# Performance work log

Hardware: AMD Instinct MI355X
Metric: run time of the kernel (lower is better)

## Reference

```python
import jax, jax.numpy as jnp
import numpy as np

N_NODES = 50000
N_EDGES = 800000
NUM_MOL = 2000
MSG_PASSES = 4


def setup_inputs() -> dict:
    key = jax.random.key(0)
    ks = jax.random.split(key, 16)
    x = jax.random.randint(ks[0], (N_NODES,), 0, 119)
    edge_attr = jax.random.randint(ks[1], (N_EDGES,), 0, 4)
    edge_index = jax.random.randint(ks[2], (2, N_EDGES), 0, N_NODES)
    batch = jnp.sort(jax.random.randint(ks[3], (N_NODES,), 0, NUM_MOL))
    f32 = jnp.float32
    return {
        "x": x,
        "edge_attr": edge_attr,
        "edge_index": edge_index,
        "batch": batch,
        "atom_table": jax.random.normal(ks[4], (119, 128), f32) * 0.1,
        "bond_table": jax.random.normal(ks[5], (4, 64), f32) * 0.1,
        "Wi": jax.random.normal(ks[6], (192, 128), f32) * 0.05,
        "bi": jax.random.normal(ks[7], (128,), f32) * 0.01,
        "Wu1": jax.random.normal(ks[8], (320, 128), f32) * 0.05,
        "bu1": jax.random.normal(ks[9], (128,), f32) * 0.01,
        "Wu2": jax.random.normal(ks[10], (128, 128), f32) * 0.05,
        "bu2": jax.random.normal(ks[11], (128,), f32) * 0.01,
        "Wr1": jax.random.normal(ks[12], (128, 512), f32) * 0.05,
        "br1": jax.random.normal(ks[13], (512,), f32) * 0.01,
        "Wr2": jax.random.normal(ks[14], (512, 1), f32) * 0.05,
        "br2": jax.random.normal(ks[15], (1,), f32) * 0.01,
    }


def reference(x, edge_attr, edge_index, batch,
              atom_table, bond_table, Wi, bi, Wu1, bu1, Wu2, bu2,
              Wr1, br1, Wr2, br2):
    atom = atom_table[x]                      # [N, atom_emb]
    bond = bond_table[edge_attr]              # [E, bond_emb]
    src, dst = edge_index[0], edge_index[1]
    a_src = atom[src]                         # [E, atom_emb]
    ab = jnp.concatenate([a_src, bond], axis=1)  # [E, atom_emb+bond_emb]
    msg = jax.nn.relu(ab @ Wi + bi)           # [E, msg_dim]
    for _ in range(MSG_PASSES):
        agg = jax.ops.segment_sum(msg, dst, num_segments=N_NODES)  # [N, msg_dim]
        upd_in = jnp.concatenate([ab, agg[src]], axis=1)           # [E, 320]
        h = jax.nn.relu(upd_in @ Wu1 + bu1)
        msg = jax.nn.relu(h @ Wu2 + bu2)
    node_state = jax.ops.segment_sum(msg, dst, num_segments=N_NODES)
    mol_state = jax.ops.segment_sum(node_state, batch, num_segments=NUM_MOL)
    out = jax.nn.relu(mol_state @ Wr1 + br1) @ Wr2 + br2  # [NUM_MOL, 1]
    return jnp.squeeze(out, axis=-1)
```

## Files before the change

kernel.cpp:

```cpp
#include <hip/hip_runtime.h>
#include <hip/hip_bf16.h>

#define N_NODES 50000
#define N_EDGES 800000
#define NUM_MOL 2000

typedef __attribute__((ext_vector_type(8))) short short8;
typedef __attribute__((ext_vector_type(4))) float f32x4;

union bfbits { __hip_bfloat16 b; short s; };

__global__ void k_tables(const float* __restrict__ atom_table,
                         const float* __restrict__ bond_table,
                         const float* __restrict__ Wi,
                         const float* __restrict__ bi,
                         const float* __restrict__ Wu1,
                         const float* __restrict__ bu1,
                         float* __restrict__ T1, float* __restrict__ U1,
                         float* __restrict__ T2c, float* __restrict__ U2c) {
  int b = blockIdx.x;
  int c = threadIdx.x;
  if (b < 119) {
    float t = 0.f, u = 0.f;
    for (int k = 0; k < 128; k++) {
      float a = atom_table[b * 128 + k];
      t += a * Wi[k * 128 + c];
      u += a * Wu1[k * 128 + c];
    }
    T1[b * 128 + c] = t;
    U1[b * 128 + c] = u;
  } else {
    int a = b - 119;
    float t = bi[c], u = bu1[c];
    for (int k = 0; k < 64; k++) {
      float bv = bond_table[a * 64 + k];
      t += bv * Wi[(128 + k) * 128 + c];
      u += bv * Wu1[(128 + k) * 128 + c];
    }
    T2c[a * 128 + c] = t;
    U2c[a * 128 + c] = u;
  }
}

__global__ void k_tt(const float* __restrict__ T1, const float* __restrict__ T2c,
                     float* __restrict__ TT) {
  int r = blockIdx.x;
  int c = threadIdx.x;
  float v = T1[(r >> 2) * 128 + c] + T2c[(r & 3) * 128 + c];
  TT[r * 128 + c] = v > 0.f ? v : 0.f;
}

__global__ void k_wt2(const float* __restrict__ Wu2, const float* __restrict__ Wu1,
                      short* __restrict__ Wt, short* __restrict__ Wlo,
                      short* __restrict__ W1t, short* __restrict__ W1lo) {
  int b = blockIdx.x;
  int k = threadIdx.x;
  if (b < 128) {
    float w = Wu2[k * 128 + b];
    bfbits hi; hi.b = __float2bfloat16(w);
    float hf = __bfloat162float(hi.b);
    bfbits lo; lo.b = __float2bfloat16(w - hf);
    Wt[b * 128 + k] = hi.s;
    Wlo[b * 128 + k] = lo.s;
  } else {
    int n = b - 128;
    float w = Wu1[(192 + k) * 128 + n];
    bfbits hi; hi.b = __float2bfloat16(w);
    float hf = __bfloat162float(hi.b);
    bfbits lo; lo.b = __float2bfloat16(w - hf);
    W1t[n * 128 + k] = hi.s;
    W1lo[n * 128 + k] = lo.s;
  }
}

__global__ void k_u1x(const int* __restrict__ x, const float* __restrict__ U1,
                      float* __restrict__ D_) {
  int n = blockIdx.x * 4 + (threadIdx.x >> 6);
  int lane = threadIdx.x & 63;
  int xn = x[n];
  float2 v = *(const float2*)&U1[xn * 128 + lane * 2];
  *(float2*)&D_[n * 128 + lane * 2] = v;
}

__global__ void k_fillb(const int* __restrict__ eidx, const int* __restrict__ attr,
                        const int* __restrict__ x,
                        int* __restrict__ cnt, int* __restrict__ csr1) {
  int e = blockIdx.x * 256 + threadIdx.x;
  int d = eidx[N_EDGES + e];
  int s = eidx[e];
  int a = attr[e];
  int pos = atomicAdd(&cnt[d], 1);
  if (pos < 64) {
    int packed = (s * 4 + a) | ((x[s] * 4 + a) << 18);
    __builtin_nontemporal_store(packed, &csr1[d * 64 + pos]);
  }
}

__global__ void k_molptr(const int* __restrict__ batch, int* __restrict__ molptr) {
  int m = blockIdx.x * 256 + threadIdx.x;
  if (m > NUM_MOL) return;
  int lo = 0, hi = N_NODES;
  while (lo < hi) {
    int mid = (lo + hi) >> 1;
    if (batch[mid] < m) lo = mid + 1; else hi = mid;
  }
  molptr[m] = lo;
}

__global__ void k_gather0(const int* __restrict__ cnt, const int* __restrict__ csr1,
                          const float* __restrict__ TT, float* __restrict__ A_) {
  int n = blockIdx.x * 4 + (threadIdx.x >> 6);
  int lane = threadIdx.x & 63;
  int g = lane >> 5;
  int p = lane & 31;
  int beg = n * 64;
  int end = beg + cnt[n];
  float s0 = 0.f, s1 = 0.f, s2 = 0.f, s3 = 0.f;
  int i = beg;
  for (; i + 3 < end; i += 4) {
    int idxA = ((unsigned)csr1[i + g]) >> 18;
    int idxB = ((unsigned)csr1[i + 2 + g]) >> 18;
    float4 va = *(const float4*)&TT[idxA * 128 + p * 4];
    float4 vb = *(const float4*)&TT[idxB * 128 + p * 4];
    s0 += va.x + vb.x; s1 += va.y + vb.y;
    s2 += va.z + vb.z; s3 += va.w + vb.w;
  }
  for (; i < end; i += 2) {
    if (i + g < end) {
      int idx = ((unsigned)csr1[i + g]) >> 18;
      float4 v = *(const float4*)&TT[idx * 128 + p * 4];
      s0 += v.x; s1 += v.y; s2 += v.z; s3 += v.w;
    }
  }
  s0 += __shfl_xor(s0, 32, 64);
  s1 += __shfl_xor(s1, 32, 64);
  s2 += __shfl_xor(s2, 32, 64);
  s3 += __shfl_xor(s3, 32, 64);
  float2 o;
  o.x = (g == 0) ? s0 : s2;
  o.y = (g == 0) ? s1 : s3;
  *(float2*)&A_[n * 128 + p * 4 + g * 2] = o;
}

__global__ void k_gather(const int* __restrict__ cnt, const int* __restrict__ csr1,
                         const __hip_bfloat16* __restrict__ M, float* __restrict__ A_) {
  int n = blockIdx.x * 4 + (threadIdx.x >> 6);
  int lane = threadIdx.x & 63;
  int g = lane >> 4;
  int p = lane & 15;
  int beg = n * 64;
  int end = beg + cnt[n];
  float s[8];
#pragma unroll
  for (int j = 0; j < 8; j++) s[j] = 0.f;
  const short* Ms = (const short*)M;
  int i = beg;
  for (; i + 7 < end; i += 8) {
    int idxA = csr1[i + g] & 0x3FFFF;
    int idxB = csr1[i + 4 + g] & 0x3FFFF;
    short8 va = *(const short8*)&Ms[idxA * 128 + p * 8];
    short8 vb = *(const short8*)&Ms[idxB * 128 + p * 8];
#pragma unroll
    for (int j = 0; j < 4; j++) {
      float2 fa = __bfloat1622float2(*(const __hip_bfloat162*)&((const short*)&va)[j * 2]);
      float2 fb = __bfloat1622float2(*(const __hip_bfloat162*)&((const short*)&vb)[j * 2]);
      s[j * 2] += fa.x + fb.x;
      s[j * 2 + 1] += fa.y + fb.y;
    }
  }
  for (; i < end; i += 4) {
    if (i + g < end) {
      int idx = csr1[i + g] & 0x3FFFF;
      short8 va = *(const short8*)&Ms[idx * 128 + p * 8];
#pragma unroll
      for (int j = 0; j < 4; j++) {
        float2 fa = __bfloat1622float2(*(const __hip_bfloat162*)&((const short*)&va)[j * 2]);
        s[j * 2] += fa.x;
        s[j * 2 + 1] += fa.y;
      }
    }
  }
#pragma unroll
  for (int j = 0; j < 8; j++) s[j] += __shfl_xor(s[j], 16, 64);
#pragma unroll
  for (int j = 0; j < 8; j++) s[j] += __shfl_xor(s[j], 32, 64);
  float2 o;
  o.x = s[g * 2];
  o.y = s[g * 2 + 1];
  *(float2*)&A_[n * 128 + p * 8 + g * 2] = o;
}

__global__ __launch_bounds__(256, 2) void k_mm1m(const float* __restrict__ A_,
                                                 const short* __restrict__ W1t,
                                                 const short* __restrict__ W1lo,
                                                 const float* __restrict__ D_,
                                                 float* __restrict__ B2_) {
  __shared__ float mbuf[4][16][68];
  int t = threadIdx.x;
  int lane = t & 63;
  int m = lane & 15;
  int quad = lane >> 4;
  int wslot = t >> 6;
  int w0 = blockIdx.x * 4 + wslot;
  int h = w0 & 1;

  short8 whi[4][4], wlo[4][4];
#pragma unroll
  for (int kc = 0; kc < 4; kc++)
#pragma unroll
    for (int nt = 0; nt < 4; nt++) {
      int n = h * 64 + nt * 16 + m;
      whi[kc][nt] = *(const short8*)&W1t[n * 128 + kc * 32 + quad * 8];
      wlo[kc][nt] = *(const short8*)&W1lo[n * 128 + kc * 32 + quad * 8];
    }

  for (int tid = w0; tid < 6250; tid += 4096) {
    int s = tid >> 1;
    int row = s * 16 + m;
    f32x4 acc[4];
#pragma unroll
    for (int nt = 0; nt < 4; nt++) acc[nt] = (f32x4){0.f, 0.f, 0.f, 0.f};

#pragma unroll
    for (int kc = 0; kc < 4; kc++) {
      int k0 = kc * 32 + quad * 8;
      short8 ahi, alo;
      {
        float av[8];
        *(float4*)&av[0] = *(const float4*)&A_[row * 128 + k0];
        *(float4*)&av[4] = *(const float4*)&A_[row * 128 + k0 + 4];
#pragma unroll
        for (int j = 0; j < 8; j++) {
          float hv = av[j];
          bfbits hi; hi.b = __float2bfloat16(hv);
          float hf = __bfloat162float(hi.b);
          bfbits lo; lo.b = __float2bfloat16(hv - hf);
          ahi[j] = hi.s;
          alo[j] = lo.s;
        }
      }
#pragma unroll
      for (int nt = 0; nt < 4; nt++) {
        acc[nt] = __builtin_amdgcn_mfma_f32_16x16x32_bf16(ahi, whi[kc][nt], acc[nt], 0, 0, 0);
        acc[nt] = __builtin_amdgcn_mfma_f32_16x16x32_bf16(alo, whi[kc][nt], acc[nt], 0, 0, 0);
        acc[nt] = __builtin_amdgcn_mfma_f32_16x16x32_bf16(ahi, wlo[kc][nt], acc[nt], 0, 0, 0);
      }
    }

#pragma unroll
    for (int nt = 0; nt < 4; nt++)
#pragma unroll
      for (int r = 0; r < 4; r++)
        mbuf[wslot][quad * 4 + r][nt * 16 + m] = acc[nt][r];
#pragma unroll
    for (int p = 0; p < 4; p++) {
      int c = p * 64 + lane;
      int rr = c >> 4;
      int qf = c & 15;
      int n = s * 16 + rr;
      float4 v = *(const float4*)&mbuf[wslot][rr][qf * 4];
      float4 d = *(const float4*)&D_[n * 128 + h * 64 + qf * 4];
      v.x += d.x; v.y += d.y; v.z += d.z; v.w += d.w;
      *(float4*)&B2_[n * 128 + h * 64 + qf * 4] = v;
    }
  }
}

__global__ __launch_bounds__(256, 2) void k_mm2(const float* __restrict__ B2_,
                                                const float* __restrict__ U2c,
                                                const short* __restrict__ Wt,
                                                const short* __restrict__ Wlo,
                                                const float* __restrict__ bu2,
                                                __hip_bfloat16* __restrict__ M) {
  __shared__ short mbuf[4][16][68];
  int t = threadIdx.x;
  int lane = t & 63;
  int m = lane & 15;
  int quad = lane >> 4;
  int wslot = t >> 6;
  int w0 = blockIdx.x * 4 + wslot;
  int h = w0 & 1;

  short8 whi[4][4], wlo[4][4];
#pragma unroll
  for (int kc = 0; kc < 4; kc++)
#pragma unroll
    for (int nt = 0; nt < 4; nt++) {
      int n = h * 64 + nt * 16 + m;
      whi[kc][nt] = *(const short8*)&Wt[n * 128 + kc * 32 + quad * 8];
      wlo[kc][nt] = *(const short8*)&Wlo[n * 128 + kc * 32 + quad * 8];
    }
  float bias[4];
#pragma unroll
  for (int nt = 0; nt < 4; nt++) bias[nt] = bu2[h * 64 + nt * 16 + m];

  for (int tid = w0; tid < 25000; tid += 4096) {
    int s = tid >> 1;
    int node = s * 4 + (m >> 2);
    int attr = m & 3;
    f32x4 acc[4];
#pragma unroll
    for (int nt = 0; nt < 4; nt++) acc[nt] = (f32x4){0.f, 0.f, 0.f, 0.f};

#pragma unroll
    for (int kc = 0; kc < 4; kc++) {
      int k0 = kc * 32 + quad * 8;
      short8 ahi, alo;
      {
        float bba[8], u2a[8];
        *(float4*)&bba[0] = *(const float4*)&B2_[node * 128 + k0];
        *(float4*)&bba[4] = *(const float4*)&B2_[node * 128 + k0 + 4];
        *(float4*)&u2a[0] = *(const float4*)&U2c[attr * 128 + k0];
        *(float4*)&u2a[4] = *(const float4*)&U2c[attr * 128 + k0 + 4];
#pragma unroll
        for (int j = 0; j < 8; j++) {
          float hv = bba[j] + u2a[j];
          hv = hv > 0.f ? hv : 0.f;
          bfbits hi; hi.b = __float2bfloat16(hv);
          float hf = __bfloat162float(hi.b);
          bfbits lo; lo.b = __float2bfloat16(hv - hf);
          ahi[j] = hi.s;
          alo[j] = lo.s;
        }
      }
#pragma unroll
      for (int nt = 0; nt < 4; nt++) {
        acc[nt] = __builtin_amdgcn_mfma_f32_16x16x32_bf16(ahi, whi[kc][nt], acc[nt], 0, 0, 0);
        acc[nt] = __builtin_amdgcn_mfma_f32_16x16x32_bf16(alo, whi[kc][nt], acc[nt], 0, 0, 0);
        acc[nt] = __builtin_amdgcn_mfma_f32_16x16x32_bf16(ahi, wlo[kc][nt], acc[nt], 0, 0, 0);
      }
    }

#pragma unroll
    for (int nt = 0; nt < 4; nt++) {
#pragma unroll
      for (int r = 0; r < 4; r++) {
        float v = acc[nt][r] + bias[nt];
        v = v > 0.f ? v : 0.f;
        bfbits o; o.b = __float2bfloat16(v);
        mbuf[wslot][quad * 4 + r][nt * 16 + m] = o.s;
      }
    }
    {
      int rr = lane >> 2;
      int qq = lane & 3;
      short8 v = *(const short8*)&mbuf[wslot][rr][qq * 8];
      *(short8*)((short*)M + (s * 16 + rr) * 128 + h * 64 + qq * 8) = v;
      short8 v2 = *(const short8*)&mbuf[wslot][rr][(qq + 4) * 8];
      *(short8*)((short*)M + (s * 16 + rr) * 128 + h * 64 + (qq + 4) * 8) = v2;
    }
  }
}

__global__ void k_molgather(const float* __restrict__ A_, const int* __restrict__ molptr,
                            float* __restrict__ mol) {
  int m = blockIdx.x * 4 + (threadIdx.x >> 6);
  int lane = threadIdx.x & 63;
  int beg = molptr[m], end = molptr[m + 1];
  float ax = 0.f, ay = 0.f;
  int n = beg;
  for (; n + 1 < end; n += 2) {
    float2 v0 = *(const float2*)&A_[n * 128 + lane * 2];
    float2 v1 = *(const float2*)&A_[(n + 1) * 128 + lane * 2];
    ax += v0.x + v1.x;
    ay += v0.y + v1.y;
  }
  if (n < end) {
    float2 v0 = *(const float2*)&A_[n * 128 + lane * 2];
    ax += v0.x;
    ay += v0.y;
  }
  float2 o; o.x = ax; o.y = ay;
  *(float2*)&mol[m * 128 + lane * 2] = o;
}

__global__ __launch_bounds__(256) void k_readout(const float* __restrict__ mol,
                                                 const float* __restrict__ Wr1,
                                                 const float* __restrict__ br1,
                                                 const float* __restrict__ Wr2,
                                                 const float* __restrict__ br2,
                                                 float* __restrict__ out) {
  int m = blockIdx.x;
  __shared__ float ms[128];
  __shared__ float red[256];
  int t = threadIdx.x;
  if (t < 128) ms[t] = mol[m * 128 + t];
  __syncthreads();
  float part = 0.f;
#pragma unroll
  for (int jj = 0; jj < 2; jj++) {
    int j = t + jj * 256;
    float acc = br1[j];
#pragma unroll
    for (int k = 0; k < 128; k += 4) {
      float4 m4 = *(const float4*)&ms[k];
      acc += m4.x * Wr1[k * 512 + j] + m4.y * Wr1[(k + 1) * 512 + j] +
             m4.z * Wr1[(k + 2) * 512 + j] + m4.w * Wr1[(k + 3) * 512 + j];
    }
    acc = acc > 0.f ? acc : 0.f;
    part += acc * Wr2[j];
  }
  red[t] = part;
  __syncthreads();
  for (int s = 128; s > 0; s >>= 1) {
    if (t < s) red[t] += red[t + s];
    __syncthreads();
  }
  if (t == 0) out[m] = red[0] + br2[0];
}

extern "C" void kernel_launch(void* const* d_in, const int* in_sizes, int n_in,
                              void* d_out, int out_size, void* d_ws, size_t ws_size,
                              hipStream_t stream) {
  const int* x        = (const int*)d_in[0];
  const int* eattr    = (const int*)d_in[1];
  const int* eidx     = (const int*)d_in[2];
  const int* batch    = (const int*)d_in[3];
  const float* atom_table = (const float*)d_in[4];
  const float* bond_table = (const float*)d_in[5];
  const float* Wi  = (const float*)d_in[6];
  const float* bi  = (const float*)d_in[7];
  const float* Wu1 = (const float*)d_in[8];
  const float* bu1 = (const float*)d_in[9];
  const float* Wu2 = (const float*)d_in[10];
  const float* bu2 = (const float*)d_in[11];
  const float* Wr1 = (const float*)d_in[12];
  const float* br1 = (const float*)d_in[13];
  const float* Wr2 = (const float*)d_in[14];
  const float* br2 = (const float*)d_in[15];
  float* out = (float*)d_out;

  char* ws = (char*)d_ws;
  __hip_bfloat16* M = (__hip_bfloat16*)(ws);
  short* Wt      = (short*)(ws + 51200000);
  short* Wlo     = (short*)(ws + 51232768);
  short* W1t     = (short*)(ws + 51265536);
  short* W1lo    = (short*)(ws + 51298304);
  int*   molptr  = (int*)  (ws + 51331072);
  int*   cnt     = (int*)  (ws + 51340000);
  int*   csr1    = (int*)  (ws + 52000000);
  float* D       = (float*)(ws + 65000000);
  float* A       = (float*)(ws + 102400000);
  float* B2      = (float*)(ws + 128000000);
  float* T1      = (float*)(ws + 157000064);
  float* U1      = (float*)(ws + 157060992);
  float* T2c     = (float*)(ws + 157121920);
  float* U2c     = (float*)(ws + 157123968);
  float* TT      = (float*)(ws + 157126016);
  float* mol     = (float*)(ws + 157369728);

  hipMemsetAsync(cnt, 0, N_NODES * sizeof(int), stream);
  k_tables<<<123, 128, 0, stream>>>(atom_table, bond_table, Wi, bi, Wu1, bu1,
                                    T1, U1, T2c, U2c);
  k_tt<<<476, 128, 0, stream>>>(T1, T2c, TT);
  k_wt2<<<256, 128, 0, stream>>>(Wu2, Wu1, Wt, Wlo, W1t, W1lo);
  k_u1x<<<N_NODES / 4, 256, 0, stream>>>(x, U1, D);
  k_fillb<<<N_EDGES / 256, 256, 0, stream>>>(eidx, eattr, x, cnt, csr1);
  k_molptr<<<(NUM_MOL + 256) / 256, 256, 0, stream>>>(batch, molptr);

  k_gather0<<<N_NODES / 4, 256, 0, stream>>>(cnt, csr1, TT, A);

  for (int p = 0; p < 4; p++) {
    k_mm1m<<<1024, 256, 0, stream>>>(A, W1t, W1lo, D, B2);
    k_mm2<<<1024, 256, 0, stream>>>(B2, U2c, Wt, Wlo, bu2, M);
    k_gather<<<N_NODES / 4, 256, 0, stream>>>(cnt, csr1, M, A);
  }

  k_molgather<<<NUM_MOL / 4, 256, 0, stream>>>(A, molptr, mol);
  k_readout<<<NUM_MOL, 256, 0, stream>>>(mol, Wr1, br1, Wr2, br2, out);
}
```

Before: 650.7 us.

## Merge prep kernels, deepen gather unrolling, raise MFMA kernel occupancy

Folds the TT-table and weight-split prep kernels into one launch to cut a kernel launch. Adds a deeper unrolled path to both gather kernels so more independent row loads are in flight per iteration. Doubles the grid and raises launch_bounds min-blocks to 4 for the two MFMA matmul kernels, which increases occupancy. The higher occupancy target may cap registers and cause spills, because each wave holds 32 short8 weight fragments in registers.

```diff
diff --git a/kernel.cpp b/kernel.cpp
--- a/kernel.cpp
+++ b/kernel.cpp
@@ -42,28 +42,26 @@
   }
 }
 
-__global__ void k_tt(const float* __restrict__ T1, const float* __restrict__ T2c,
-                     float* __restrict__ TT) {
-  int r = blockIdx.x;
-  int c = threadIdx.x;
-  float v = T1[(r >> 2) * 128 + c] + T2c[(r & 3) * 128 + c];
-  TT[r * 128 + c] = v > 0.f ? v : 0.f;
-}
-
-__global__ void k_wt2(const float* __restrict__ Wu2, const float* __restrict__ Wu1,
-                      short* __restrict__ Wt, short* __restrict__ Wlo,
-                      short* __restrict__ W1t, short* __restrict__ W1lo) {
+__global__ void k_prep(const float* __restrict__ T1, const float* __restrict__ T2c,
+                       const float* __restrict__ Wu2, const float* __restrict__ Wu1,
+                       float* __restrict__ TT,
+                       short* __restrict__ Wt, short* __restrict__ Wlo,
+                       short* __restrict__ W1t, short* __restrict__ W1lo) {
   int b = blockIdx.x;
   int k = threadIdx.x;
-  if (b < 128) {
-    float w = Wu2[k * 128 + b];
+  if (b < 476) {
+    float v = T1[(b >> 2) * 128 + k] + T2c[(b & 3) * 128 + k];
+    TT[b * 128 + k] = v > 0.f ? v : 0.f;
+  } else if (b < 604) {
+    int n = b - 476;
+    float w = Wu2[k * 128 + n];
     bfbits hi; hi.b = __float2bfloat16(w);
     float hf = __bfloat162float(hi.b);
     bfbits lo; lo.b = __float2bfloat16(w - hf);
-    Wt[b * 128 + k] = hi.s;
-    Wlo[b * 128 + k] = lo.s;
+    Wt[n * 128 + k] = hi.s;
+    Wlo[n * 128 + k] = lo.s;
   } else {
-    int n = b - 128;
+    int n = b - 604;
     float w = Wu1[(192 + k) * 128 + n];
     bfbits hi; hi.b = __float2bfloat16(w);
     float hf = __bfloat162float(hi.b);
@@ -117,11 +115,25 @@
   int end = beg + cnt[n];
   float s0 = 0.f, s1 = 0.f, s2 = 0.f, s3 = 0.f;
   int i = beg;
+  for (; i + 7 < end; i += 8) {
+    int iA = ((unsigned)csr1[i + g]) >> 18;
+    int iB = ((unsigned)csr1[i + 2 + g]) >> 18;
+    int iC = ((unsigned)csr1[i + 4 + g]) >> 18;
+    int iD = ((unsigned)csr1[i + 6 + g]) >> 18;
+    float4 va = *(const float4*)&TT[iA * 128 + p * 4];
+    float4 vb = *(const float4*)&TT[iB * 128 + p * 4];
+    float4 vc = *(const float4*)&TT[iC * 128 + p * 4];
+    float4 vd = *(const float4*)&TT[iD * 128 + p * 4];
+    s0 += (va.x + vb.x) + (vc.x + vd.x);
+    s1 += (va.y + vb.y) + (vc.y + vd.y);
+    s2 += (va.z + vb.z) + (vc.z + vd.z);
+    s3 += (va.w + vb.w) + (vc.w + vd.w);
+  }
   for (; i + 3 < end; i += 4) {
-    int idxA = ((unsigned)csr1[i + g]) >> 18;
-    int idxB = ((unsigned)csr1[i + 2 + g]) >> 18;
-    float4 va = *(const float4*)&TT[idxA * 128 + p * 4];
-    float4 vb = *(const float4*)&TT[idxB * 128 + p * 4];
+    int iA = ((unsigned)csr1[i + g]) >> 18;
+    int iB = ((unsigned)csr1[i + 2 + g]) >> 18;
+    float4 va = *(const float4*)&TT[iA * 128 + p * 4];
+    float4 vb = *(const float4*)&TT[iB * 128 + p * 4];
     s0 += va.x + vb.x; s1 += va.y + vb.y;
     s2 += va.z + vb.z; s3 += va.w + vb.w;
   }
@@ -155,11 +167,30 @@
   for (int j = 0; j < 8; j++) s[j] = 0.f;
   const short* Ms = (const short*)M;
   int i = beg;
+  for (; i + 15 < end; i += 16) {
+    int iA = csr1[i + g] & 0x3FFFF;
+    int iB = csr1[i + 4 + g] & 0x3FFFF;
+    int iC = csr1[i + 8 + g] & 0x3FFFF;
+    int iD = csr1[i + 12 + g] & 0x3FFFF;
+    short8 va = *(const short8*)&Ms[iA * 128 + p * 8];
+    short8 vb = *(const short8*)&Ms[iB * 128 + p * 8];
+    short8 vc = *(const short8*)&Ms[iC * 128 + p * 8];
+    short8 vd = *(const short8*)&Ms[iD * 128 + p * 8];
+#pragma unroll
+    for (int j = 0; j < 4; j++) {
+      float2 fa = __bfloat1622float2(*(const __hip_bfloat162*)&((const short*)&va)[j * 2]);
+      float2 fb = __bfloat1622float2(*(const __hip_bfloat162*)&((const short*)&vb)[j * 2]);
+      float2 fc = __bfloat1622float2(*(const __hip_bfloat162*)&((const short*)&vc)[j * 2]);
+      float2 fd = __bfloat1622float2(*(const __hip_bfloat162*)&((const short*)&vd)[j * 2]);
+      s[j * 2] += (fa.x + fb.x) + (fc.x + fd.x);
+      s[j * 2 + 1] += (fa.y + fb.y) + (fc.y + fd.y);
+    }
+  }
   for (; i + 7 < end; i += 8) {
-    int idxA = csr1[i + g] & 0x3FFFF;
-    int idxB = csr1[i + 4 + g] & 0x3FFFF;
-    short8 va = *(const short8*)&Ms[idxA * 128 + p * 8];
-    short8 vb = *(const short8*)&Ms[idxB * 128 + p * 8];
+    int iA = csr1[i + g] & 0x3FFFF;
+    int iB = csr1[i + 4 + g] & 0x3FFFF;
+    short8 va = *(const short8*)&Ms[iA * 128 + p * 8];
+    short8 vb = *(const short8*)&Ms[iB * 128 + p * 8];
 #pragma unroll
     for (int j = 0; j < 4; j++) {
       float2 fa = __bfloat1622float2(*(const __hip_bfloat162*)&((const short*)&va)[j * 2]);
@@ -190,7 +221,7 @@
   *(float2*)&A_[n * 128 + p * 8 + g * 2] = o;
 }
 
-__global__ __launch_bounds__(256, 2) void k_mm1m(const float* __restrict__ A_,
+__global__ __launch_bounds__(256, 4) void k_mm1m(const float* __restrict__ A_,
                                                  const short* __restrict__ W1t,
                                                  const short* __restrict__ W1lo,
                                                  const float* __restrict__ D_,
@@ -214,7 +245,7 @@
       wlo[kc][nt] = *(const short8*)&W1lo[n * 128 + kc * 32 + quad * 8];
     }
 
-  for (int tid = w0; tid < 6250; tid += 4096) {
+  for (int tid = w0; tid < 6250; tid += 8192) {
     int s = tid >> 1;
     int row = s * 16 + m;
     f32x4 acc[4];
@@ -266,7 +297,7 @@
   }
 }
 
-__global__ __launch_bounds__(256, 2) void k_mm2(const float* __restrict__ B2_,
+__global__ __launch_bounds__(256, 4) void k_mm2(const float* __restrict__ B2_,
                                                 const float* __restrict__ U2c,
                                                 const short* __restrict__ Wt,
                                                 const short* __restrict__ Wlo,
@@ -294,7 +325,7 @@
 #pragma unroll
   for (int nt = 0; nt < 4; nt++) bias[nt] = bu2[h * 64 + nt * 16 + m];
 
-  for (int tid = w0; tid < 25000; tid += 4096) {
+  for (int tid = w0; tid < 25000; tid += 8192) {
     int s = tid >> 1;
     int node = s * 4 + (m >> 2);
     int attr = m & 3;
@@ -452,8 +483,7 @@
   hipMemsetAsync(cnt, 0, N_NODES * sizeof(int), stream);
   k_tables<<<123, 128, 0, stream>>>(atom_table, bond_table, Wi, bi, Wu1, bu1,
                                     T1, U1, T2c, U2c);
-  k_tt<<<476, 128, 0, stream>>>(T1, T2c, TT);
-  k_wt2<<<256, 128, 0, stream>>>(Wu2, Wu1, Wt, Wlo, W1t, W1lo);
+  k_prep<<<732, 128, 0, stream>>>(T1, T2c, Wu2, Wu1, TT, Wt, Wlo, W1t, W1lo);
   k_u1x<<<N_NODES / 4, 256, 0, stream>>>(x, U1, D);
   k_fillb<<<N_EDGES / 256, 256, 0, stream>>>(eidx, eattr, x, cnt, csr1);
   k_molptr<<<(NUM_MOL + 256) / 256, 256, 0, stream>>>(batch, molptr);
@@ -461,8 +491,8 @@
   k_gather0<<<N_NODES / 4, 256, 0, stream>>>(cnt, csr1, TT, A);
 
   for (int p = 0; p < 4; p++) {
-    k_mm1m<<<1024, 256, 0, stream>>>(A, W1t, W1lo, D, B2);
-    k_mm2<<<1024, 256, 0, stream>>>(B2, U2c, Wt, Wlo, bu2, M);
+    k_mm1m<<<2048, 256, 0, stream>>>(A, W1t, W1lo, D, B2);
+    k_mm2<<<2048, 256, 0, stream>>>(B2, U2c, Wt, Wlo, bu2, M);
     k_gather<<<N_NODES / 4, 256, 0, stream>>>(cnt, csr1, M, A);
   }
 
```

Result: slower. 1.045 ms (+60.6%).
